# Optimization experiments

Measured on AMD Instinct MI355X. Metric: run time of the kernel, lower is better.

The kernel has to match this reference:

```python
import jax, jax.numpy as jnp
import numpy as np

N_NODES = 49
FEAT_DIM = 1280            # efficientnet_v2_s feature dim
NODE_DIM = FEAT_DIM // N_NODES  # 26
GAT_HID = 256
HEADS = 4
NUM_CLASSES = 5
BATCH = 8192


def _grid_edges():
    # 7x7 grid, 8-neighborhood, as in _create_grid_edges, plus PyG default self loops
    edges = []
    for i in range(7):
        for j in range(7):
            node = i * 7 + j
            for di in (-1, 0, 1):
                for dj in (-1, 0, 1):
                    if di == 0 and dj == 0:
                        continue
                    ni, nj = i + di, j + dj
                    if 0 <= ni < 7 and 0 <= nj < 7:
                        edges.append((node, ni * 7 + nj))
    edges += [(n, n) for n in range(N_NODES)]  # add_self_loops=True (PyG default)
    return np.asarray(edges, dtype=np.int64).T  # [2, 361]


def setup_inputs() -> dict:
    key = jax.random.key(0)
    ks = jax.random.split(key, 16)
    s = 0.05
    inp = {
        "x": jax.random.normal(ks[0], (BATCH, FEAT_DIM), jnp.float32),
        "transform_w": jax.random.normal(ks[1], (FEAT_DIM, N_NODES * NODE_DIM), jnp.float32) * s,
        "transform_b": jnp.zeros((N_NODES * NODE_DIM,), jnp.float32),
        # GATv2 layer 1: 26 -> 64 per head, 4 heads, concat -> 256
        "g1_wl": jax.random.normal(ks[2], (NODE_DIM, GAT_HID), jnp.float32) * s,
        "g1_wr": jax.random.normal(ks[3], (NODE_DIM, GAT_HID), jnp.float32) * s,
        "g1_att": jax.random.normal(ks[4], (HEADS, GAT_HID // HEADS), jnp.float32) * s,
        "g1_b": jnp.zeros((GAT_HID,), jnp.float32),
        # GATv2 layer 2: 256 -> 256, 1 head, mean
        "g2_wl": jax.random.normal(ks[5], (GAT_HID, GAT_HID), jnp.float32) * s,
        "g2_wr": jax.random.normal(ks[6], (GAT_HID, GAT_HID), jnp.float32) * s,
        "g2_att": jax.random.normal(ks[7], (1, GAT_HID), jnp.float32) * s,
        "g2_b": jnp.zeros((GAT_HID,), jnp.float32),
        "fc_w": jax.random.normal(ks[8], (NODE_DIM + GAT_HID, NUM_CLASSES), jnp.float32) * s,
        "fc_b": jnp.zeros((NUM_CLASSES,), jnp.float32),
        "edge_index": jnp.asarray(_grid_edges()),
    }
    return inp


def _gatv2(x, src, dst, wl, wr, att, b, heads, out_ch, concat):
    # PyG GATv2Conv (share_weights=False, negative_slope=0.2, eval mode)
    n = x.shape[0]
    xl = (x @ wl).reshape(n, heads, out_ch)  # source messages
    xr = (x @ wr).reshape(n, heads, out_ch)  # target side of attention
    e = jax.nn.leaky_relu(xl[src] + xr[dst], 0.2)        # [E, H, C]
    score = jnp.einsum('ehc,hc->eh', e, att)             # [E, H]
    smax = jax.ops.segment_max(score, dst, num_segments=n)
    ex = jnp.exp(score - smax[dst])
    den = jax.ops.segment_sum(ex, dst, num_segments=n)
    alpha = ex / den[dst]                                # softmax over in-edges per node
    out = jax.ops.segment_sum(xl[src] * alpha[..., None], dst, num_segments=n)  # [N,H,C]
    out = out.reshape(n, heads * out_ch) if concat else out.mean(axis=1)
    return out + b


def reference(x, transform_w, transform_b, g1_wl, g1_wr, g1_att, g1_b,
              g2_wl, g2_wr, g2_att, g2_b, fc_w, fc_b, edge_index):
    src, dst = edge_index[0], edge_index[1]
    node = (x @ transform_w + transform_b).reshape(-1, N_NODES, NODE_DIM)  # [B,49,26]

    def graph(nf):
        h = _gatv2(nf, src, dst, g1_wl, g1_wr, g1_att, g1_b, HEADS, GAT_HID // HEADS, True)
        h = jax.nn.elu(h)  # dropout inactive in eval
        h = _gatv2(h, src, dst, g2_wl, g2_wr, g2_att, g2_b, 1, GAT_HID, False)
        return h  # [49, 256]

    g = jax.vmap(graph)(node)                              # [B,49,256]
    pooled = jnp.concatenate([node, g], axis=-1).mean(axis=1)  # [B, 282]
    return pooled @ fc_w + fc_b
```

## Files before the change

kernel.cpp:

```cpp
#include <hip/hip_runtime.h>
#include <hip/hip_bf16.h>

typedef __bf16 bf16;
typedef __attribute__((ext_vector_type(8))) __bf16 bf16x8;
typedef __attribute__((ext_vector_type(4))) float f32x4;

constexpr int BATCH = 8192, NN = 49, ND = 26, NOUT = 1274, FD = 1280;
constexpr int HID = 256, NE = 361, HEADS = 4;
constexpr int KT_X = 40;
constexpr int MT_X = 512;
constexpr int NT_X = 80;

constexpr size_t OFF_XPACK = 0;
constexpr size_t SZ_XPACK  = (size_t)MT_X * KT_X * 512 * 2;
constexpr size_t OFF_WPACK = OFF_XPACK + SZ_XPACK;
constexpr size_t SZ_WPACK  = (size_t)NT_X * KT_X * 512 * 2;
constexpr size_t OFF_B1    = OFF_WPACK + SZ_WPACK;
constexpr size_t SZ_B1     = (size_t)32 * 512 * 2;
constexpr size_t OFF_B2    = OFF_B1 + SZ_B1;
constexpr size_t SZ_B2     = (size_t)32 * 8 * 512 * 2;
constexpr size_t OFF_A1    = OFF_B2 + SZ_B2;
constexpr size_t SZ_A1     = (size_t)(BATCH * NN / 16) * 512 * 2;
constexpr size_t OFF_PN    = OFF_A1 + SZ_A1;
constexpr size_t SZ_PN     = (size_t)BATCH * ND * 4;
constexpr size_t OFF_CSR   = OFF_PN + SZ_PN;
constexpr size_t SZ_CSR    = 8192;
constexpr size_t OFF_CHUNK = OFF_CSR + SZ_CSR;


__global__ __launch_bounds__(256) void k_pack_x(const float* __restrict__ x,
                                                bf16* __restrict__ xp) {
    int g = blockIdx.x * 256 + threadIdx.x;
    int lane = g & 63, frag = g >> 6;
    int mt = frag / KT_X, kt = frag - mt * KT_X;
    int row = mt * 16 + (lane & 15);
    int k0  = kt * 32 + (lane >> 4) * 8;
    const float* src = x + (size_t)row * FD + k0;
    bf16x8 v;
#pragma unroll
    for (int j = 0; j < 8; ++j) v[j] = (bf16)src[j];
    *(bf16x8*)(xp + ((size_t)frag * 64 + lane) * 8) = v;
}

__global__ __launch_bounds__(256) void k_pack_w(const float* __restrict__ w,
                                                bf16* __restrict__ wp) {
    int g = blockIdx.x * 256 + threadIdx.x;
    int lane = g & 63, frag = g >> 6;
    int nt = frag / KT_X, kt = frag - nt * KT_X;
    int col = nt * 16 + (lane & 15);
    int k0  = kt * 32 + (lane >> 4) * 8;
    bf16x8 v;
#pragma unroll
    for (int j = 0; j < 8; ++j)
        v[j] = (col < NOUT) ? (bf16)w[(size_t)(k0 + j) * NOUT + col] : (bf16)0.f;
    *(bf16x8*)(wp + ((size_t)frag * 64 + lane) * 8) = v;
}

__global__ __launch_bounds__(256) void k_pack_g1(const float* __restrict__ wl,
                                                 const float* __restrict__ wr,
                                                 bf16* __restrict__ bp) {
    int g = blockIdx.x * 256 + threadIdx.x;
    int lane = g & 63, nt = g >> 6;
    int n  = nt * 16 + (lane & 15);
    int k0 = (lane >> 4) * 8;
    bf16x8 v;
#pragma unroll
    for (int j = 0; j < 8; ++j) {
        int k = k0 + j;
        float f = 0.f;
        if (k < ND) f = (n < HID) ? wl[k * HID + n] : wr[k * HID + (n - HID)];
        v[j] = (bf16)f;
    }
    *(bf16x8*)(bp + ((size_t)nt * 64 + lane) * 8) = v;
}

__global__ __launch_bounds__(256) void k_pack_g2(const float* __restrict__ wl,
                                                 const float* __restrict__ wr,
                                                 bf16* __restrict__ bp) {
    int g = blockIdx.x * 256 + threadIdx.x;
    int lane = g & 63, frag = g >> 6;
    int nt = frag >> 3, kt = frag & 7;
    int n  = nt * 16 + (lane & 15);
    int k0 = kt * 32 + (lane >> 4) * 8;
    bf16x8 v;
#pragma unroll
    for (int j = 0; j < 8; ++j) {
        int k = k0 + j;
        float f = (n < HID) ? wl[k * HID + n] : wr[k * HID + (n - HID)];
        v[j] = (bf16)f;
    }
    *(bf16x8*)(bp + ((size_t)frag * 64 + lane) * 8) = v;
}

__global__ __launch_bounds__(128) void k_csr_par(const int* __restrict__ ei,
                                                 int* __restrict__ csr) {
    __shared__ int es[NE], ed[NE], cnt[NN], ocnt[NN], off[NN + 1], ooff[NN + 1];
    int tid = threadIdx.x;
    if (tid < NN) { cnt[tid] = 0; ocnt[tid] = 0; }
    for (int e = tid; e < NE; e += 128) { es[e] = ei[e]; ed[e] = ei[NE + e]; }
    __syncthreads();
    for (int e = tid; e < NE; e += 128) {
        atomicAdd(&cnt[ed[e]], 1);
        atomicAdd(&ocnt[es[e]], 1);
    }
    __syncthreads();
    if (tid == 0) {
        off[0] = 0; ooff[0] = 0;
        for (int n = 0; n < NN; ++n) {
            off[n + 1] = off[n] + cnt[n];
            ooff[n + 1] = ooff[n] + ocnt[n];
        }
    }
    __syncthreads();
    if (tid < NN) {
        int p = off[tid];
        for (int e = 0; e < NE; ++e)
            if (ed[e] == tid) { csr[50 + p] = e; csr[411 + p] = es[e]; ++p; }
    } else if (tid >= 64 && tid < 64 + NN) {
        int n = tid - 64;
        int p = ooff[n];
        for (int e = 0; e < NE; ++e)
            if (es[e] == n) { csr[822 + p] = e; ++p; }
    }
    if (tid < 50) { csr[tid] = off[tid]; csr[772 + tid] = ooff[tid]; }
}

__global__ __launch_bounds__(256) void k_gemm_node(const bf16* __restrict__ xp,
                                                   const bf16* __restrict__ wp,
                                                   const float* __restrict__ tb,
                                                   bf16* __restrict__ A1,
                                                   float* __restrict__ pooledN) {
    int tid = threadIdx.x, lane = tid & 63, w = tid >> 6;
    int mtb = blockIdx.x * 8 + (w >> 1) * 4;
    int ntb = blockIdx.y * 8 + (w & 1) * 4;
    f32x4 acc[4][4] = {};
    for (int kt = 0; kt < KT_X; ++kt) {
        bf16x8 a[4], b[4];
#pragma unroll
        for (int i = 0; i < 4; ++i)
            a[i] = *(const bf16x8*)(xp + (((size_t)(mtb + i) * KT_X + kt) * 64 + lane) * 8);
#pragma unroll
        for (int j = 0; j < 4; ++j)
            b[j] = *(const bf16x8*)(wp + (((size_t)(ntb + j) * KT_X + kt) * 64 + lane) * 8);
#pragma unroll
        for (int i = 0; i < 4; ++i)
#pragma unroll
            for (int j = 0; j < 4; ++j)
                acc[i][j] = __builtin_amdgcn_mfma_f32_16x16x32_bf16(a[i], b[j], acc[i][j], 0, 0, 0);
    }
    int c0 = lane & 15, r0 = (lane >> 4) * 4;
#pragma unroll
    for (int j = 0; j < 4; ++j) {
        int col = (ntb + j) * 16 + c0;
        if (col >= NOUT) continue;
        float bias = tb[col];
        int n = col / 26, d = col - n * 26;
#pragma unroll
        for (int i = 0; i < 4; ++i) {
            int rowb = (mtb + i) * 16 + r0;
#pragma unroll
            for (int r = 0; r < 4; ++r) {
                int brow = rowb + r;
                float val = acc[i][j][r] + bias;
                int R = brow * NN + n;
                A1[(((size_t)(R >> 4)) * 64 + ((d >> 3) << 4) + (R & 15)) * 8 + (d & 7)] = (bf16)val;
                atomicAdd(&pooledN[brow * ND + d], val);
            }
        }
    }
}

template<int KT>
__global__ __launch_bounds__(256) void k_gemm_gat(const bf16* __restrict__ Af,
                                                  const bf16* __restrict__ Bf,
                                                  char* __restrict__ xlr) {
    int tid = threadIdx.x, lane = tid & 63, w = tid >> 6;
    int mtb = blockIdx.x * 8 + (w >> 1) * 4;
    int ntb = blockIdx.y * 8 + (w & 1) * 4;
    f32x4 acc[4][4] = {};
    for (int kt = 0; kt < KT; ++kt) {
        bf16x8 a[4], b[4];
#pragma unroll
        for (int i = 0; i < 4; ++i)
            a[i] = *(const bf16x8*)(Af + (((size_t)(mtb + i) * KT + kt) * 64 + lane) * 8);
#pragma unroll
        for (int j = 0; j < 4; ++j)
            b[j] = *(const bf16x8*)(Bf + (((size_t)(ntb + j) * KT + kt) * 64 + lane) * 8);
#pragma unroll
        for (int i = 0; i < 4; ++i)
#pragma unroll
            for (int j = 0; j < 4; ++j)
                acc[i][j] = __builtin_amdgcn_mfma_f32_16x16x32_bf16(a[i], b[j], acc[i][j], 0, 0, 0);
    }
    int c0 = lane & 15, r0 = (lane >> 4) * 4;
#pragma unroll
    for (int i = 0; i < 4; ++i) {
        int Rbase = (mtb + i) * 16 + r0;
        int lr0 = Rbase % NN;
#pragma unroll
        for (int r = 0; r < 4; ++r) {
            int R = Rbase + r;
            int lr = lr0 + r; if (lr >= NN) lr -= NN;
            char* rowp = xlr + (size_t)R * 1024;
            int sw = (lr & 7) << 4;
#pragma unroll
            for (int j = 0; j < 4; ++j) {
                int col = (ntb + j) * 16 + c0;
                *(bf16*)(rowp + ((col * 2) ^ sw)) = (bf16)acc[i][j][r];
            }
        }
    }
}

__global__ __launch_bounds__(512, 4) void k_edge1(const char* __restrict__ xlrG,
                                                  bf16* __restrict__ h1f,
                                                  const float* __restrict__ att1,
                                                  const float* __restrict__ g1b,
                                                  const int* __restrict__ ei,
                                                  const int* __restrict__ csr) {
    __shared__ __align__(16) char X[NN * 1024];
    __shared__ __align__(16) float attS[256];
    __shared__ float sc[NE * 4], srden[NN * 4], bS[256];
    __shared__ int srcS[NE], dstS[NE], ieOff[50], ieId[NE], ieSrc[NE];

    int tid = threadIdx.x, g = blockIdx.x;
    const char* srcp = xlrG + (size_t)g * (NN * 1024);
    for (int off = tid * 16; off < NN * 1024; off += 512 * 16)
        *(uint4*)(X + off) = *(const uint4*)(srcp + off);
    for (int i = tid; i < 256; i += 512) { attS[i] = att1[i]; bS[i] = g1b[i]; }
    for (int i = tid; i < NE; i += 512) {
        srcS[i] = ei[i]; dstS[i] = ei[NE + i];
        ieId[i] = csr[50 + i]; ieSrc[i] = csr[411 + i];
    }
    if (tid < 50) ieOff[tid] = csr[tid];
    __syncthreads();

    int rot = tid & 7;
    for (int task = tid; task < NE * 4; task += 512) {
        int h = task / NE, e = task - h * NE;
        int s = srcS[e], d = dstS[e];
        int sws = (s & 7) << 4, swd = (d & 7) << 4;
        const char* ps = X + s * 1024;
        const char* pd = X + d * 1024;
        float p = 0.f;
#pragma unroll
        for (int i = 0; i < 8; ++i) {
            int cc = ((i + rot) & 7) * 8;
            bf16x8 xl = *(const bf16x8*)(ps + (((h * 64 + cc) * 2) ^ sws));
            bf16x8 xr = *(const bf16x8*)(pd + (((256 + h * 64 + cc) * 2) ^ swd));
            float4 a0 = *(const float4*)(attS + h * 64 + cc);
            float4 a1 = *(const float4*)(attS + h * 64 + cc + 4);
            const float aa[8] = {a0.x, a0.y, a0.z, a0.w, a1.x, a1.y, a1.z, a1.w};
#pragma unroll
            for (int q = 0; q < 8; ++q) {
                float v = (float)xl[q] + (float)xr[q];
                v = v > 0.f ? v : 0.2f * v;
                p = fmaf(aa[q], v, p);
            }
        }
        sc[e * 4 + h] = p;
    }
    __syncthreads();
    for (int t = tid; t < NN * 4; t += 512) {
        int n = t >> 2, h = t & 3;
        float m = -1e30f;
        for (int j = ieOff[n]; j < ieOff[n + 1]; ++j) m = fmaxf(m, sc[ieId[j] * 4 + h]);
        float den = 0.f;
        for (int j = ieOff[n]; j < ieOff[n + 1]; ++j) {
            int idx = ieId[j] * 4 + h;
            float ex = __expf(sc[idx] - m);
            sc[idx] = ex; den += ex;
        }
        srden[t] = 1.f / den;
    }
    __syncthreads();
    int gbase = g * NN;
    for (int task = tid; task < NN * 32; task += 512) {
        int n = task >> 5, cb = task & 31;
        int ch0 = cb * 8, hh = cb >> 3;
        float a8[8] = {};
        int j0 = ieOff[n], j1 = ieOff[n + 1];
        for (int j = j0; j < j1; ++j) {
            float al = sc[ieId[j] * 4 + hh];
            int s = ieSrc[j];
            bf16x8 xv = *(const bf16x8*)(X + s * 1024 + ((ch0 * 2) ^ ((s & 7) << 4)));
#pragma unroll
            for (int q = 0; q < 8; ++q) a8[q] = fmaf(al, (float)xv[q], a8[q]);
        }
        float rs = srden[n * 4 + hh];
        int Rl = gbase + n;
        bf16x8 o;
#pragma unroll
        for (int q = 0; q < 8; ++q) {
            float v = fmaf(a8[q], rs, bS[ch0 + q]);
            v = v > 0.f ? v : (__expf(v) - 1.f);
            o[q] = (bf16)v;
        }
        size_t addr = (((size_t)(Rl >> 4) * 8 + (ch0 >> 5)) * 64 + ((ch0 >> 3) & 3) * 16 + (Rl & 15)) * 8;
        *(bf16x8*)(h1f + addr) = o;
    }
}

static __device__ __forceinline__ float waveReduceSum(float v) {
#pragma unroll
    for (int m = 32; m > 0; m >>= 1) v += __shfl_xor(v, m, 64);
    return v;
}

__global__ __launch_bounds__(512, 4) void k_edge2(const char* __restrict__ xlrG,
                                                  const float* __restrict__ pooledN,
                                                  const float* __restrict__ att2,
                                                  const float* __restrict__ g2b,
                                                  const float* __restrict__ fcw,
                                                  const float* __restrict__ fcb,
                                                  const int* __restrict__ ei,
                                                  const int* __restrict__ csr,
                                                  int graph_base,
                                                  float* __restrict__ out) {
    __shared__ __align__(16) char X[NN * 1024];
    __shared__ __align__(16) float attS[256];
    __shared__ float sc2[NE * 2], scE[NE], srdenN[NN], smaxN[NN], wS[NN];
    __shared__ float b2S[256], pA[256], pB[256], pool[288], fcwS[282 * 5];
    __shared__ int srcS[NE], dstS[NE], ieOff[50], ieId[NE], oOff[50], oId[NE];

    int tid = threadIdx.x, g = blockIdx.x;
    const char* srcp = xlrG + (size_t)g * (NN * 1024);
    for (int off = tid * 16; off < NN * 1024; off += 512 * 16)
        *(uint4*)(X + off) = *(const uint4*)(srcp + off);
    for (int i = tid; i < 256; i += 512) { attS[i] = att2[i]; b2S[i] = g2b[i]; }
    for (int i = tid; i < NE; i += 512) {
        srcS[i] = ei[i]; dstS[i] = ei[NE + i];
        ieId[i] = csr[50 + i]; oId[i] = csr[822 + i];
    }
    if (tid < 50) { ieOff[tid] = csr[tid]; oOff[tid] = csr[772 + tid]; }
    for (int i = tid; i < 282 * 5; i += 512) fcwS[i] = fcw[i];
    __syncthreads();

    int rot = tid & 7;
    for (int task = tid; task < NE * 2; task += 512) {
        int e = task >> 1, half = task & 1;
        int s = srcS[e], d = dstS[e];
        int sws = (s & 7) << 4, swd = (d & 7) << 4;
        const char* ps = X + s * 1024;
        const char* pd = X + d * 1024;
        float p = 0.f;
#pragma unroll
        for (int i = 0; i < 16; ++i) {
            int cc = half * 128 + (((i + rot) & 15)) * 8;
            bf16x8 xl = *(const bf16x8*)(ps + ((cc * 2) ^ sws));
            bf16x8 xr = *(const bf16x8*)(pd + (((256 + cc) * 2) ^ swd));
            float4 a0 = *(const float4*)(attS + cc);
            float4 a1 = *(const float4*)(attS + cc + 4);
            const float aa[8] = {a0.x, a0.y, a0.z, a0.w, a1.x, a1.y, a1.z, a1.w};
#pragma unroll
            for (int q = 0; q < 8; ++q) {
                float v = (float)xl[q] + (float)xr[q];
                v = v > 0.f ? v : 0.2f * v;
                p = fmaf(aa[q], v, p);
            }
        }
        sc2[task] = p;
    }
    __syncthreads();
    for (int e = tid; e < NE; e += 512) scE[e] = sc2[2 * e] + sc2[2 * e + 1];
    __syncthreads();
    for (int n = tid; n < NN; n += 512) {
        float m = -1e30f;
        for (int j = ieOff[n]; j < ieOff[n + 1]; ++j) m = fmaxf(m, scE[ieId[j]]);
        float den = 0.f;
        for (int j = ieOff[n]; j < ieOff[n + 1]; ++j) den += __expf(scE[ieId[j]] - m);
        smaxN[n] = m; srdenN[n] = 1.f / den;
    }
    __syncthreads();
    for (int n = tid; n < NN; n += 512) {
        float wacc = 0.f;
        for (int j = oOff[n]; j < oOff[n + 1]; ++j) {
            int e = oId[j], d = dstS[e];
            wacc += __expf(scE[e] - smaxN[d]) * srdenN[d];
        }
        wS[n] = wacc;
    }
    __syncthreads();
    {
        int ch = tid & 255, half = tid >> 8;
        int n0 = half ? 25 : 0, n1 = half ? NN : 25;
        float acc = 0.f;
        for (int n = n0; n < n1; ++n) {
            float v = (float)*(const bf16*)(X + n * 1024 + ((ch * 2) ^ ((n & 7) << 4)));
            acc = fmaf(wS[n], v, acc);
        }
        (half ? pB : pA)[ch] = acc;
    }
    __syncthreads();
    if (tid < ND) pool[tid] = pooledN[(size_t)(graph_base + g) * ND + tid] * (1.f / NN);
    else if (tid >= 32 && tid < 32 + HID) {
        int ch = tid - 32;
        pool[ND + ch] = (pA[ch] + pB[ch]) * (1.f / NN) + b2S[ch];
    }
    __syncthreads();
    int w5 = tid >> 6, lane = tid & 63;
    if (w5 < 5) {
        float a = 0.f;
        for (int d = lane; d < ND + HID; d += 64) a = fmaf(pool[d], fcwS[d * 5 + w5], a);
        a = waveReduceSum(a);
        if (lane == 0) out[(size_t)(graph_base + g) * 5 + w5] = a + fcb[w5];
    }
}

extern "C" void kernel_launch(void* const* d_in, const int* in_sizes, int n_in,
                              void* d_out, int out_size, void* d_ws, size_t ws_size,
                              hipStream_t stream) {
    const float* x   = (const float*)d_in[0];
    const float* tw  = (const float*)d_in[1];
    const float* tb  = (const float*)d_in[2];
    const float* wl1 = (const float*)d_in[3];
    const float* wr1 = (const float*)d_in[4];
    const float* at1 = (const float*)d_in[5];
    const float* b1  = (const float*)d_in[6];
    const float* wl2 = (const float*)d_in[7];
    const float* wr2 = (const float*)d_in[8];
    const float* at2 = (const float*)d_in[9];
    const float* b2  = (const float*)d_in[10];
    const float* fcw = (const float*)d_in[11];
    const float* fcb = (const float*)d_in[12];
    const int*   ei  = (const int*)d_in[13];
    float* out = (float*)d_out;

    char* ws = (char*)d_ws;
    bf16*  xp   = (bf16*)(ws + OFF_XPACK);
    bf16*  wp   = (bf16*)(ws + OFF_WPACK);
    bf16*  b1p  = (bf16*)(ws + OFF_B1);
    bf16*  b2p  = (bf16*)(ws + OFF_B2);
    bf16*  A1   = (bf16*)(ws + OFF_A1);
    float* pN   = (float*)(ws + OFF_PN);
    int*   csr  = (int*)(ws + OFF_CSR);

    int C = 128;
    for (int cand : {2048, 1024, 512, 256, 128}) {
        if (OFF_CHUNK + (size_t)cand * (50176 + 25088) <= ws_size) { C = cand; break; }
    }
    char* xlr = ws + OFF_CHUNK;
    bf16* h1f = (bf16*)(ws + OFF_CHUNK + (size_t)C * 50176);
    int nchunks = BATCH / C;
    int MtC = C * NN / 16;

    hipMemsetAsync(A1, 0, SZ_A1, stream);
    hipMemsetAsync(pN, 0, SZ_PN, stream);

    k_pack_x<<<dim3(MT_X * KT_X * 64 / 256), dim3(256), 0, stream>>>(x, xp);
    k_pack_w<<<dim3(NT_X * KT_X * 64 / 256), dim3(256), 0, stream>>>(tw, wp);
    k_pack_g1<<<dim3(8), dim3(256), 0, stream>>>(wl1, wr1, b1p);
    k_pack_g2<<<dim3(64), dim3(256), 0, stream>>>(wl2, wr2, b2p);
    k_csr_par<<<dim3(1), dim3(128), 0, stream>>>(ei, csr);
    k_gemm_node<<<dim3(64, 10), dim3(256), 0, stream>>>(xp, wp, tb, A1, pN);

    for (int c = 0; c < nchunks; ++c) {
        const bf16* A1c = A1 + (size_t)c * MtC * 512;
        k_gemm_gat<1><<<dim3(MtC / 8, 4), dim3(256), 0, stream>>>(A1c, b1p, xlr);
        k_edge1<<<dim3(C), dim3(512), 0, stream>>>(xlr, h1f, at1, b1, ei, csr);
        k_gemm_gat<8><<<dim3(MtC / 8, 4), dim3(256), 0, stream>>>(h1f, b2p, xlr);
        k_edge2<<<dim3(C), dim3(512), 0, stream>>>(xlr, pN, at2, b2, fcw, fcb, ei, csr,
                                                   c * C, out);
    }
}
```

Measured before the change: 1.024 ms.

## Node-aligned node GEMM tiling, drop atomics, per-node softmax in edge1

The node-transform GEMM is retiled so each block covers whole nodes (130 columns, 9 n-tiles). Results are staged through shared memory and written as a dense padded [B,49,32] bf16 layout, replacing the scattered stores and the per-element atomicAdd pooling. Pooling moves to a separate reduction kernel, so the memsets are no longer needed. edge1 now computes scores and softmax per destination node in registers, storing only normalized alphas, and launch bounds and the maximum chunk size are lowered. The extra pool kernel and the larger register footprint are the tradeoffs.

```diff
diff --git a/kernel.cpp b/kernel.cpp
--- a/kernel.cpp
+++ b/kernel.cpp
@@ -9,19 +9,20 @@
 constexpr int HID = 256, NE = 361, HEADS = 4;
 constexpr int KT_X = 40;
 constexpr int MT_X = 512;
-constexpr int NT_X = 80;
+constexpr int NB_W = 10;
+constexpr int NTB  = 9;
 
 constexpr size_t OFF_XPACK = 0;
 constexpr size_t SZ_XPACK  = (size_t)MT_X * KT_X * 512 * 2;
 constexpr size_t OFF_WPACK = OFF_XPACK + SZ_XPACK;
-constexpr size_t SZ_WPACK  = (size_t)NT_X * KT_X * 512 * 2;
+constexpr size_t SZ_WPACK  = (size_t)NB_W * NTB * KT_X * 512 * 2;
 constexpr size_t OFF_B1    = OFF_WPACK + SZ_WPACK;
 constexpr size_t SZ_B1     = (size_t)32 * 512 * 2;
 constexpr size_t OFF_B2    = OFF_B1 + SZ_B1;
 constexpr size_t SZ_B2     = (size_t)32 * 8 * 512 * 2;
-constexpr size_t OFF_A1    = OFF_B2 + SZ_B2;
-constexpr size_t SZ_A1     = (size_t)(BATCH * NN / 16) * 512 * 2;
-constexpr size_t OFF_PN    = OFF_A1 + SZ_A1;
+constexpr size_t OFF_N32   = OFF_B2 + SZ_B2;
+constexpr size_t SZ_N32    = (size_t)BATCH * NN * 32 * 2;
+constexpr size_t OFF_PN    = OFF_N32 + SZ_N32;
 constexpr size_t SZ_PN     = (size_t)BATCH * ND * 4;
 constexpr size_t OFF_CSR   = OFF_PN + SZ_PN;
 constexpr size_t SZ_CSR    = 8192;
@@ -46,13 +47,15 @@
                                                 bf16* __restrict__ wp) {
     int g = blockIdx.x * 256 + threadIdx.x;
     int lane = g & 63, frag = g >> 6;
-    int nt = frag / KT_X, kt = frag - nt * KT_X;
-    int col = nt * 16 + (lane & 15);
+    int kt = frag % KT_X, t2 = frag / KT_X;
+    int nt = t2 % NTB, nb = t2 / NTB;
+    int col = nb * 130 + nt * 16 + (lane & 15);
     int k0  = kt * 32 + (lane >> 4) * 8;
+    bool ok = (col < NOUT) && (col < nb * 130 + 130);
     bf16x8 v;
 #pragma unroll
     for (int j = 0; j < 8; ++j)
-        v[j] = (col < NOUT) ? (bf16)w[(size_t)(k0 + j) * NOUT + col] : (bf16)0.f;
+        v[j] = ok ? (bf16)w[(size_t)(k0 + j) * NOUT + col] : (bf16)0.f;
     *(bf16x8*)(wp + ((size_t)frag * 64 + lane) * 8) = v;
 }
 
@@ -128,70 +131,88 @@
 __global__ __launch_bounds__(256) void k_gemm_node(const bf16* __restrict__ xp,
                                                    const bf16* __restrict__ wp,
                                                    const float* __restrict__ tb,
-                                                   bf16* __restrict__ A1,
-                                                   float* __restrict__ pooledN) {
+                                                   bf16* __restrict__ node32) {
+    __shared__ bf16 L[128][148];
+    __shared__ float tbS[144];
+    int tid = threadIdx.x, lane = tid & 63, w = tid >> 6;
+    int nb = blockIdx.y, C0 = nb * 130;
+    int mt0 = blockIdx.x * 8 + w * 2;
+    if (tid < 144) { int col = C0 + tid; tbS[tid] = (col < NOUT) ? tb[col] : 0.f; }
+    f32x4 acc[2][9] = {};
+    const bf16* wpB = wp + (size_t)(nb * NTB) * KT_X * 512;
+    for (int kt = 0; kt < KT_X; ++kt) {
+        bf16x8 a[2];
+#pragma unroll
+        for (int i = 0; i < 2; ++i)
+            a[i] = *(const bf16x8*)(xp + (((size_t)(mt0 + i) * KT_X + kt) * 64 + lane) * 8);
+#pragma unroll
+        for (int j = 0; j < NTB; ++j) {
+            bf16x8 b = *(const bf16x8*)(wpB + ((size_t)(j * KT_X + kt) * 64 + lane) * 8);
+            acc[0][j] = __builtin_amdgcn_mfma_f32_16x16x32_bf16(a[0], b, acc[0][j], 0, 0, 0);
+            acc[1][j] = __builtin_amdgcn_mfma_f32_16x16x32_bf16(a[1], b, acc[1][j], 0, 0, 0);
+        }
+    }
+    __syncthreads();
+    int c0 = lane & 15, r0 = (lane >> 4) * 4;
+#pragma unroll
+    for (int i = 0; i < 2; ++i) {
+        int rowb = (w * 2 + i) * 16 + r0;
+#pragma unroll
+        for (int j = 0; j < NTB; ++j) {
+            int col = j * 16 + c0;
+            float bias = tbS[col];
+#pragma unroll
+            for (int r = 0; r < 4; ++r)
+                L[rowb + r][col] = (bf16)(acc[i][j][r] + bias);
+        }
+    }
+    __syncthreads();
+    int nodes = (nb == 9) ? 4 : 5;
+    int total = 128 * nodes * 4;
+    int B0 = blockIdx.x * 128;
+    for (int t = tid; t < total; t += 256) {
+        int q = t & 3, t2 = t >> 2;
+        int n_l = t2 % nodes, brow = t2 / nodes;
+        bf16x8 o;
+#pragma unroll
+        for (int jj = 0; jj < 8; ++jj) {
+            int d = q * 8 + jj;
+            o[jj] = (d < ND) ? L[brow][n_l * 26 + d] : (bf16)0.f;
+        }
+        *(bf16x8*)(node32 + (((size_t)(B0 + brow) * NN + nb * 5 + n_l) * 32 + q * 8)) = o;
+    }
+}
+
+__global__ __launch_bounds__(256) void k_pool(const bf16* __restrict__ node32,
+                                              float* __restrict__ pN) {
+    int b = blockIdx.x * 8 + (threadIdx.x >> 5);
+    int d = threadIdx.x & 31;
+    if (d >= ND) return;
+    const bf16* base = node32 + (size_t)b * NN * 32 + d;
+    float s = 0.f;
+    for (int n = 0; n < NN; ++n) s += (float)base[n * 32];
+    pN[b * ND + d] = s;
+}
+
+__global__ __launch_bounds__(256) void k_gemm_l1(const bf16* __restrict__ n32,
+                                                 const bf16* __restrict__ Bf,
+                                                 char* __restrict__ xlr) {
     int tid = threadIdx.x, lane = tid & 63, w = tid >> 6;
     int mtb = blockIdx.x * 8 + (w >> 1) * 4;
     int ntb = blockIdx.y * 8 + (w & 1) * 4;
     f32x4 acc[4][4] = {};
-    for (int kt = 0; kt < KT_X; ++kt) {
-        bf16x8 a[4], b[4];
-#pragma unroll
-        for (int i = 0; i < 4; ++i)
-            a[i] = *(const bf16x8*)(xp + (((size_t)(mtb + i) * KT_X + kt) * 64 + lane) * 8);
+    bf16x8 a[4], b[4];
+#pragma unroll
+    for (int i = 0; i < 4; ++i)
+        a[i] = *(const bf16x8*)(n32 + ((size_t)((mtb + i) * 16 + (lane & 15))) * 32 + (lane >> 4) * 8);
+#pragma unroll
+    for (int j = 0; j < 4; ++j)
+        b[j] = *(const bf16x8*)(Bf + ((size_t)(ntb + j) * 64 + lane) * 8);
+#pragma unroll
+    for (int i = 0; i < 4; ++i)
 #pragma unroll
         for (int j = 0; j < 4; ++j)
-            b[j] = *(const bf16x8*)(wp + (((size_t)(ntb + j) * KT_X + kt) * 64 + lane) * 8);
-#pragma unroll
-        for (int i = 0; i < 4; ++i)
-#pragma unroll
-            for (int j = 0; j < 4; ++j)
-                acc[i][j] = __builtin_amdgcn_mfma_f32_16x16x32_bf16(a[i], b[j], acc[i][j], 0, 0, 0);
-    }
-    int c0 = lane & 15, r0 = (lane >> 4) * 4;
-#pragma unroll
-    for (int j = 0; j < 4; ++j) {
-        int col = (ntb + j) * 16 + c0;
-        if (col >= NOUT) continue;
-        float bias = tb[col];
-        int n = col / 26, d = col - n * 26;
-#pragma unroll
-        for (int i = 0; i < 4; ++i) {
-            int rowb = (mtb + i) * 16 + r0;
-#pragma unroll
-            for (int r = 0; r < 4; ++r) {
-                int brow = rowb + r;
-                float val = acc[i][j][r] + bias;
-                int R = brow * NN + n;
-                A1[(((size_t)(R >> 4)) * 64 + ((d >> 3) << 4) + (R & 15)) * 8 + (d & 7)] = (bf16)val;
-                atomicAdd(&pooledN[brow * ND + d], val);
-            }
-        }
-    }
-}
-
-template<int KT>
-__global__ __launch_bounds__(256) void k_gemm_gat(const bf16* __restrict__ Af,
-                                                  const bf16* __restrict__ Bf,
-                                                  char* __restrict__ xlr) {
-    int tid = threadIdx.x, lane = tid & 63, w = tid >> 6;
-    int mtb = blockIdx.x * 8 + (w >> 1) * 4;
-    int ntb = blockIdx.y * 8 + (w & 1) * 4;
-    f32x4 acc[4][4] = {};
-    for (int kt = 0; kt < KT; ++kt) {
-        bf16x8 a[4], b[4];
-#pragma unroll
-        for (int i = 0; i < 4; ++i)
-            a[i] = *(const bf16x8*)(Af + (((size_t)(mtb + i) * KT + kt) * 64 + lane) * 8);
-#pragma unroll
-        for (int j = 0; j < 4; ++j)
-            b[j] = *(const bf16x8*)(Bf + (((size_t)(ntb + j) * KT + kt) * 64 + lane) * 8);
-#pragma unroll
-        for (int i = 0; i < 4; ++i)
-#pragma unroll
-            for (int j = 0; j < 4; ++j)
-                acc[i][j] = __builtin_amdgcn_mfma_f32_16x16x32_bf16(a[i], b[j], acc[i][j], 0, 0, 0);
-    }
+            acc[i][j] = __builtin_amdgcn_mfma_f32_16x16x32_bf16(a[i], b[j], acc[i][j], 0, 0, 0);
     int c0 = lane & 15, r0 = (lane >> 4) * 4;
 #pragma unroll
     for (int i = 0; i < 4; ++i) {
@@ -212,66 +233,109 @@
     }
 }
 
-__global__ __launch_bounds__(512, 4) void k_edge1(const char* __restrict__ xlrG,
+__global__ __launch_bounds__(256) void k_gemm_l2(const bf16* __restrict__ Af,
+                                                 const bf16* __restrict__ Bf,
+                                                 char* __restrict__ xlr) {
+    int tid = threadIdx.x, lane = tid & 63, w = tid >> 6;
+    int mtb = blockIdx.x * 8 + (w >> 1) * 4;
+    int ntb = blockIdx.y * 8 + (w & 1) * 4;
+    f32x4 acc[4][4] = {};
+    for (int kt = 0; kt < 8; ++kt) {
+        bf16x8 a[4], b[4];
+#pragma unroll
+        for (int i = 0; i < 4; ++i)
+            a[i] = *(const bf16x8*)(Af + (((size_t)(mtb + i) * 8 + kt) * 64 + lane) * 8);
+#pragma unroll
+        for (int j = 0; j < 4; ++j)
+            b[j] = *(const bf16x8*)(Bf + (((size_t)(ntb + j) * 8 + kt) * 64 + lane) * 8);
+#pragma unroll
+        for (int i = 0; i < 4; ++i)
+#pragma unroll
+            for (int j = 0; j < 4; ++j)
+                acc[i][j] = __builtin_amdgcn_mfma_f32_16x16x32_bf16(a[i], b[j], acc[i][j], 0, 0, 0);
+    }
+    int c0 = lane & 15, r0 = (lane >> 4) * 4;
+#pragma unroll
+    for (int i = 0; i < 4; ++i) {
+        int Rbase = (mtb + i) * 16 + r0;
+        int lr0 = Rbase % NN;
+#pragma unroll
+        for (int r = 0; r < 4; ++r) {
+            int R = Rbase + r;
+            int lr = lr0 + r; if (lr >= NN) lr -= NN;
+            char* rowp = xlr + (size_t)R * 1024;
+            int sw = (lr & 7) << 4;
+#pragma unroll
+            for (int j = 0; j < 4; ++j) {
+                int col = (ntb + j) * 16 + c0;
+                *(bf16*)(rowp + ((col * 2) ^ sw)) = (bf16)acc[i][j][r];
+            }
+        }
+    }
+}
+
+constexpr int MAXD = 9;
+__global__ __launch_bounds__(512, 2) void k_edge1(const char* __restrict__ xlrG,
                                                   bf16* __restrict__ h1f,
                                                   const float* __restrict__ att1,
                                                   const float* __restrict__ g1b,
-                                                  const int* __restrict__ ei,
                                                   const int* __restrict__ csr) {
     __shared__ __align__(16) char X[NN * 1024];
-    __shared__ __align__(16) float attS[256];
-    __shared__ float sc[NE * 4], srden[NN * 4], bS[256];
-    __shared__ int srcS[NE], dstS[NE], ieOff[50], ieId[NE], ieSrc[NE];
+    __shared__ __align__(16) bf16 attB[256];
+    __shared__ float alphaS[NE * 4];
+    __shared__ float bS[256];
+    __shared__ int ieOff[50], ieSrc[NE];
 
     int tid = threadIdx.x, g = blockIdx.x;
     const char* srcp = xlrG + (size_t)g * (NN * 1024);
     for (int off = tid * 16; off < NN * 1024; off += 512 * 16)
         *(uint4*)(X + off) = *(const uint4*)(srcp + off);
-    for (int i = tid; i < 256; i += 512) { attS[i] = att1[i]; bS[i] = g1b[i]; }
-    for (int i = tid; i < NE; i += 512) {
-        srcS[i] = ei[i]; dstS[i] = ei[NE + i];
-        ieId[i] = csr[50 + i]; ieSrc[i] = csr[411 + i];
-    }
+    if (tid < 256) { attB[tid] = (bf16)att1[tid]; }
+    else if (tid < 512 && tid - 256 < 256) { bS[tid - 256] = g1b[tid - 256]; }
+    for (int i = tid; i < NE; i += 512) ieSrc[i] = csr[411 + i];
     if (tid < 50) ieOff[tid] = csr[tid];
     __syncthreads();
 
-    int rot = tid & 7;
-    for (int task = tid; task < NE * 4; task += 512) {
-        int h = task / NE, e = task - h * NE;
-        int s = srcS[e], d = dstS[e];
-        int sws = (s & 7) << 4, swd = (d & 7) << 4;
-        const char* ps = X + s * 1024;
-        const char* pd = X + d * 1024;
-        float p = 0.f;
+    if (tid < NN * HEADS) {
+        int n = tid >> 2, h = tid & 3;
+        int swd = (n & 7) << 4;
+        bf16x8 xr8[8], at8[8];
 #pragma unroll
         for (int i = 0; i < 8; ++i) {
-            int cc = ((i + rot) & 7) * 8;
-            bf16x8 xl = *(const bf16x8*)(ps + (((h * 64 + cc) * 2) ^ sws));
-            bf16x8 xr = *(const bf16x8*)(pd + (((256 + h * 64 + cc) * 2) ^ swd));
-            float4 a0 = *(const float4*)(attS + h * 64 + cc);
-            float4 a1 = *(const float4*)(attS + h * 64 + cc + 4);
-            const float aa[8] = {a0.x, a0.y, a0.z, a0.w, a1.x, a1.y, a1.z, a1.w};
-#pragma unroll
-            for (int q = 0; q < 8; ++q) {
-                float v = (float)xl[q] + (float)xr[q];
-                v = v > 0.f ? v : 0.2f * v;
-                p = fmaf(aa[q], v, p);
-            }
-        }
-        sc[e * 4 + h] = p;
-    }
-    __syncthreads();
-    for (int t = tid; t < NN * 4; t += 512) {
-        int n = t >> 2, h = t & 3;
+            xr8[i] = *(const bf16x8*)(X + n * 1024 + (((256 + h * 64 + i * 8) * 2) ^ swd));
+            at8[i] = *(const bf16x8*)(attB + h * 64 + i * 8);
+        }
+        int j0 = ieOff[n], deg = ieOff[n + 1] - j0;
+        float p[MAXD];
+#pragma unroll
+        for (int jj = 0; jj < MAXD; ++jj) {
+            if (jj < deg) {
+                int s = ieSrc[j0 + jj];
+                int sws = (s & 7) << 4;
+                float acc = 0.f;
+#pragma unroll
+                for (int i = 0; i < 8; ++i) {
+                    bf16x8 xl = *(const bf16x8*)(X + s * 1024 + (((h * 64 + i * 8) * 2) ^ sws));
+#pragma unroll
+                    for (int q = 0; q < 8; ++q) {
+                        float v = (float)xl[q] + (float)xr8[i][q];
+                        v = v > 0.f ? v : 0.2f * v;
+                        acc = fmaf((float)at8[i][q], v, acc);
+                    }
+                }
+                p[jj] = acc;
+            } else p[jj] = -1e30f;
+        }
         float m = -1e30f;
-        for (int j = ieOff[n]; j < ieOff[n + 1]; ++j) m = fmaxf(m, sc[ieId[j] * 4 + h]);
+#pragma unroll
+        for (int jj = 0; jj < MAXD; ++jj) m = fmaxf(m, p[jj]);
         float den = 0.f;
-        for (int j = ieOff[n]; j < ieOff[n + 1]; ++j) {
-            int idx = ieId[j] * 4 + h;
-            float ex = __expf(sc[idx] - m);
-            sc[idx] = ex; den += ex;
-        }
-        srden[t] = 1.f / den;
+#pragma unroll
+        for (int jj = 0; jj < MAXD; ++jj) { p[jj] = __expf(p[jj] - m); den += p[jj]; }
+        float r = 1.f / den;
+#pragma unroll
+        for (int jj = 0; jj < MAXD; ++jj)
+            if (jj < deg) alphaS[(j0 + jj) * 4 + h] = p[jj] * r;
     }
     __syncthreads();
     int gbase = g * NN;
@@ -281,18 +345,17 @@
         float a8[8] = {};
         int j0 = ieOff[n], j1 = ieOff[n + 1];
         for (int j = j0; j < j1; ++j) {
-            float al = sc[ieId[j] * 4 + hh];
+            float al = alphaS[j * 4 + hh];
             int s = ieSrc[j];
             bf16x8 xv = *(const bf16x8*)(X + s * 1024 + ((ch0 * 2) ^ ((s & 7) << 4)));
 #pragma unroll
             for (int q = 0; q < 8; ++q) a8[q] = fmaf(al, (float)xv[q], a8[q]);
         }
-        float rs = srden[n * 4 + hh];
         int Rl = gbase + n;
         bf16x8 o;
 #pragma unroll
         for (int q = 0; q < 8; ++q) {
-            float v = fmaf(a8[q], rs, bS[ch0 + q]);
+            float v = a8[q] + bS[ch0 + q];
             v = v > 0.f ? v : (__expf(v) - 1.f);
             o[q] = (bf16)v;
         }
@@ -307,7 +370,7 @@
     return v;
 }
 
-__global__ __launch_bounds__(512, 4) void k_edge2(const char* __restrict__ xlrG,
+__global__ __launch_bounds__(512, 2) void k_edge2(const char* __restrict__ xlrG,
                                                   const float* __restrict__ pooledN,
                                                   const float* __restrict__ att2,
                                                   const float* __restrict__ g2b,
@@ -431,12 +494,12 @@
     bf16*  wp   = (bf16*)(ws + OFF_WPACK);
     bf16*  b1p  = (bf16*)(ws + OFF_B1);
     bf16*  b2p  = (bf16*)(ws + OFF_B2);
-    bf16*  A1   = (bf16*)(ws + OFF_A1);
+    bf16*  n32  = (bf16*)(ws + OFF_N32);
     float* pN   = (float*)(ws + OFF_PN);
     int*   csr  = (int*)(ws + OFF_CSR);
 
     int C = 128;
-    for (int cand : {2048, 1024, 512, 256, 128}) {
+    for (int cand : {1024, 512, 256, 128}) {
         if (OFF_CHUNK + (size_t)cand * (50176 + 25088) <= ws_size) { C = cand; break; }
     }
     char* xlr = ws + OFF_CHUNK;
@@ -444,21 +507,19 @@
     int nchunks = BATCH / C;
     int MtC = C * NN / 16;
 
-    hipMemsetAsync(A1, 0, SZ_A1, stream);
-    hipMemsetAsync(pN, 0, SZ_PN, stream);
-
     k_pack_x<<<dim3(MT_X * KT_X * 64 / 256), dim3(256), 0, stream>>>(x, xp);
-    k_pack_w<<<dim3(NT_X * KT_X * 64 / 256), dim3(256), 0, stream>>>(tw, wp);
+    k_pack_w<<<dim3(NB_W * NTB * KT_X * 64 / 256), dim3(256), 0, stream>>>(tw, wp);
     k_pack_g1<<<dim3(8), dim3(256), 0, stream>>>(wl1, wr1, b1p);
     k_pack_g2<<<dim3(64), dim3(256), 0, stream>>>(wl2, wr2, b2p);
     k_csr_par<<<dim3(1), dim3(128), 0, stream>>>(ei, csr);
-    k_gemm_node<<<dim3(64, 10), dim3(256), 0, stream>>>(xp, wp, tb, A1, pN);
+    k_gemm_node<<<dim3(64, NB_W), dim3(256), 0, stream>>>(xp, wp, tb, n32);
+    k_pool<<<dim3(BATCH / 8), dim3(256), 0, stream>>>(n32, pN);
 
     for (int c = 0; c < nchunks; ++c) {
-        const bf16* A1c = A1 + (size_t)c * MtC * 512;
-        k_gemm_gat<1><<<dim3(MtC / 8, 4), dim3(256), 0, stream>>>(A1c, b1p, xlr);
-        k_edge1<<<dim3(C), dim3(512), 0, stream>>>(xlr, h1f, at1, b1, ei, csr);
-        k_gemm_gat<8><<<dim3(MtC / 8, 4), dim3(256), 0, stream>>>(h1f, b2p, xlr);
+        const bf16* n32c = n32 + (size_t)c * C * NN * 32;
+        k_gemm_l1<<<dim3(MtC / 8, 4), dim3(256), 0, stream>>>(n32c, b1p, xlr);
+        k_edge1<<<dim3(C), dim3(512), 0, stream>>>(xlr, h1f, at1, b1, csr);
+        k_gemm_l2<<<dim3(MtC / 8, 4), dim3(256), 0, stream>>>(h1f, b2p, xlr);
         k_edge2<<<dim3(C), dim3(512), 0, stream>>>(xlr, pN, at2, b2, fcw, fcb, ei, csr,
                                                    c * C, out);
     }
```

Result: slower. 1.320 ms (+28.8%).
